# Kernel optimization log

Measured on AMD Instinct MI355X. Metric: run time of the kernel, lower is better.

Reference implementation:

```python
import jax, jax.numpy as jnp
import numpy as np
from jax.ops import segment_sum

N_NODES = 100000
N_EDGES = 1600000
HIDDEN = 128


def gcn_conv(x, src, dst, w, W, b, num_nodes):
    """PyG GCNConv: add self-loops (weight 1), symmetric deg^-1/2 normalization,
    gather from src, scatter-add to dst. x: [N, Fin], W: [Fin, Fout]."""
    loop = jnp.arange(num_nodes, dtype=src.dtype)
    s = jnp.concatenate([src, loop])
    d = jnp.concatenate([dst, loop])
    ww = jnp.concatenate([w, jnp.ones((num_nodes,), dtype=w.dtype)])
    deg = segment_sum(ww, d, num_segments=num_nodes)           # [N]
    dis = jnp.where(deg > 0, jax.lax.rsqrt(jnp.where(deg > 0, deg, 1.0)), 0.0)
    norm = dis[s] * ww * dis[d]                                # [E+N]
    h = x @ W                                                  # [N, Fout]
    msg = norm[:, None] * h[s]                                 # [E+N, Fout]
    out = segment_sum(msg, d, num_segments=num_nodes)          # [N, Fout]
    return out + b


def setup_inputs() -> dict:
    key = jax.random.key(0)
    ks = jax.random.split(key, 12)
    h = HIDDEN
    sc = lambda fan_in: 1.0 / np.sqrt(fan_in)
    return {
        "x": jax.random.normal(ks[0], (N_NODES, 1), dtype=jnp.float32),
        "edge_index": jax.random.randint(ks[1], (2, N_EDGES), 0, N_NODES, dtype=jnp.int64),
        "edge_weight": jax.random.uniform(ks[2], (N_EDGES,), dtype=jnp.float32),
        "W1": jax.random.normal(ks[3], (1, h), dtype=jnp.float32) * sc(1),
        "b1": jnp.zeros((h,), dtype=jnp.float32),
        "W2": jax.random.normal(ks[4], (h, 2 * h), dtype=jnp.float32) * sc(h),
        "b2": jnp.zeros((2 * h,), dtype=jnp.float32),
        "Wl1": jax.random.normal(ks[5], (2 * h, h), dtype=jnp.float32) * sc(2 * h),
        "bl1": jnp.zeros((h,), dtype=jnp.float32),
        "Wl2": jax.random.normal(ks[6], (h, 1), dtype=jnp.float32) * sc(h),
        "bl2": jnp.zeros((1,), dtype=jnp.float32),
    }


def reference(x, edge_index, edge_weight, W1, b1, W2, b2, Wl1, bl1, Wl2, bl2):
    n = x.shape[0]
    src, dst = edge_index[0], edge_index[1]
    h = jax.nn.relu(gcn_conv(x, src, dst, edge_weight, W1, b1, n))
    h = jax.nn.relu(gcn_conv(h, src, dst, edge_weight, W2, b2, n))
    h = jax.nn.relu(h @ Wl1 + bl1)
    return h @ Wl2 + bl2
```

## Files before the change

### kernel.cpp

```cpp
#include <hip/hip_runtime.h>


#define HD 128
#define HD2 256
#define BSHIFT 8
#define BNODES 256
#define SRCBITS 17

typedef __attribute__((ext_vector_type(8))) short bf8_t;
typedef __attribute__((ext_vector_type(4))) float f32x4;

static inline size_t align256(size_t x) { return (x + 255) & ~(size_t)255; }

__device__ inline ushort f2bf(float f) {
    uint u = __float_as_uint(f);
    uint r = u + 0x7fffu + ((u >> 16) & 1u);
    return (ushort)(r >> 16);
}
__device__ inline uint packbf(float a, float b) {
    return (uint)f2bf(a) | ((uint)f2bf(b) << 16);
}

__global__ void k_init(const float* __restrict__ W2, const float* __restrict__ Wl1,
                       ushort* __restrict__ Bt1, ushort* __restrict__ Bt2,
                       int* __restrict__ bfill) {
    int o = blockIdx.x * blockDim.x + threadIdx.x;
    if (o < 512) bfill[o] = 0;
    if (o >= 32768) return;
    {
        int k0 = o & 7, n = (o >> 3) & 255, k8 = o >> 11;
        Bt1[o] = f2bf(W2[(size_t)(k8 * 8 + k0) * 256 + n]);
    }
    {
        int k0 = o & 7, n = (o >> 3) & 127, k8 = o >> 10;
        Bt2[o] = f2bf(Wl1[(size_t)(k8 * 8 + k0) * 128 + n]);
    }
}

__global__ __launch_bounds__(256) void k_part(const int* __restrict__ ei,
                                              const float* __restrict__ ew,
                                              int* __restrict__ bfill,
                                              uint2* __restrict__ stg,
                                              int E, int nbuck, int cap) {
    __shared__ int lcnt[4][512];
    __shared__ int lbase[4][512];
    int tid = threadIdx.x;
    int wvid = tid >> 6;
    for (int i = tid; i < nbuck; i += 256) {
        lcnt[0][i] = 0; lcnt[1][i] = 0; lcnt[2][i] = 0; lcnt[3][i] = 0;
    }
    __syncthreads();
    bool is64 = (ei[1] == 0) && (ei[3] == 0) && (ei[5] == 0) && (ei[7] == 0);
    int e0 = blockIdx.x * 2048;
    uint pack[8]; uint wb[8]; int bkt[8]; int rank[8];
    for (int u = 0; u < 8; u++) {
        int e = e0 + u * 256 + tid;
        bkt[u] = -1;
        if (e < E) {
            int s, d;
            if (is64) { s = ei[2 * e]; d = ei[2 * (E + e)]; }
            else      { s = ei[e];     d = ei[E + e]; }
            bkt[u] = d >> BSHIFT;
            pack[u] = ((uint)(d & (BNODES - 1)) << SRCBITS) | (uint)s;
            wb[u] = __float_as_uint(ew[e]);
            rank[u] = atomicAdd(&lcnt[wvid][bkt[u]], 1);
        }
    }
    __syncthreads();
    for (int i = tid; i < nbuck; i += 256) {
        int t0 = lcnt[0][i], t1 = lcnt[1][i], t2 = lcnt[2][i], t3 = lcnt[3][i];
        int tot = t0 + t1 + t2 + t3;
        int base = tot ? atomicAdd(&bfill[i], tot) : 0;
        lbase[0][i] = base;
        lbase[1][i] = base + t0;
        lbase[2][i] = base + t0 + t1;
        lbase[3][i] = base + t0 + t1 + t2;
    }
    __syncthreads();
    for (int u = 0; u < 8; u++)
        if (bkt[u] >= 0)
            stg[(size_t)bkt[u] * cap + lbase[wvid][bkt[u]] + rank[u]] =
                make_uint2(pack[u], wb[u]);
}

__global__ __launch_bounds__(512) void k_fine(const uint2* __restrict__ stg,
                                              const int* __restrict__ bfill,
                                              const float* __restrict__ x,
                                              float* __restrict__ dis,
                                              float* __restrict__ p,
                                              int* __restrict__ rowptr,
                                              int2* __restrict__ cv,
                                              int cap, int N, int E, int nbuck) {
    __shared__ int cnt_l[BNODES];
    __shared__ int base_l[BNODES];
    __shared__ float degf[BNODES];
    __shared__ int wsum[8];
    int b = blockIdx.x, tid = threadIdx.x;
    int lane = tid & 63, wvid = tid >> 6;
    int a = (tid < b && tid < nbuck) ? bfill[tid] : 0;
    for (int off = 32; off > 0; off >>= 1) a += __shfl_xor(a, off);
    if (lane == 0) wsum[wvid] = a;
    __syncthreads();
    int cb = wsum[0] + wsum[1] + wsum[2] + wsum[3] +
             wsum[4] + wsum[5] + wsum[6] + wsum[7];
    int n = bfill[b];
    if (b == nbuck - 1 && tid == 0) rowptr[N] = E;
    const uint2* s = stg + (size_t)b * cap;
    if (tid < BNODES) { cnt_l[tid] = 0; degf[tid] = 1.0f; }
    __syncthreads();
    for (int i = tid; i < n; i += 512)
        atomicAdd(&cnt_l[s[i].x >> SRCBITS], 1);
    __syncthreads();
    int c = 0;
    if (tid < BNODES) { c = cnt_l[tid]; cnt_l[tid] = 0; }
    int v = c;
    for (int off = 1; off < 64; off <<= 1) {
        int u = __shfl_up(v, off);
        if (lane >= off) v += u;
    }
    if (wvid < 4 && lane == 63) wsum[wvid] = v;
    __syncthreads();
    if (tid < BNODES) {
        int wpre = 0;
        for (int k = 0; k < wvid; k++) wpre += wsum[k];
        base_l[tid] = v + wpre - c;
    }
    __syncthreads();
    for (int i = tid; i < n; i += 512) {
        uint2 r = s[i];
        int dl = r.x >> SRCBITS;
        int src = (int)(r.x & ((1u << SRCBITS) - 1));
        int pos = cb + base_l[dl] + atomicAdd(&cnt_l[dl], 1);
        cv[pos] = make_int2(src, (int)r.y);
        atomicAdd(&degf[dl], __uint_as_float(r.y));
    }
    __syncthreads();
    int gid = (b << BSHIFT) + tid;
    if (tid < BNODES && gid < N) {
        rowptr[gid] = cb + base_l[tid];
        float r = rsqrtf(degf[tid]);
        dis[gid] = r;
        p[gid] = r * x[gid];
    }
}

__global__ __launch_bounds__(256) void k_q(const int* __restrict__ rowptr,
                                           const int2* __restrict__ cv,
                                           const float* __restrict__ dis,
                                           const float* __restrict__ p,
                                           float2* __restrict__ tp, int N) {
    int gid = blockIdx.x * blockDim.x + threadIdx.x;
    int wid = gid >> 4;
    int sl = threadIdx.x & 15;
    if (wid >= N) return;
    int beg = rowptr[wid], end = rowptr[wid + 1];
    float s = 0.0f;
    for (int i = beg + sl; i < end; i += 16) {
        int2 pr = cv[i];
        s += __int_as_float(pr.y) * p[pr.x];
    }
    s += __shfl_xor(s, 1);
    s += __shfl_xor(s, 2);
    s += __shfl_xor(s, 4);
    s += __shfl_xor(s, 8);
    if (sl == 0) {
        float r = dis[wid];
        tp[wid] = make_float2(r * (s + p[wid]), r);
    }
}

__global__ __launch_bounds__(256) void k_agg(const int* __restrict__ rowptr,
                                             const int2* __restrict__ cv,
                                             const float2* __restrict__ tp,
                                             const float* __restrict__ W1,
                                             const float* __restrict__ b1,
                                             uint* __restrict__ z, int N) {
    __shared__ float4 eb[4][32];
    int tid = threadIdx.x;
    int wvid = tid >> 6, lane = tid & 63;
    int wid = (blockIdx.x * blockDim.x + tid) >> 6;
    if (wid >= N) return;
    float2 w1 = *(const float2*)(W1 + lane * 2);
    float2 bb = *(const float2*)(b1 + lane * 2);
    int beg = rowptr[wid], end = rowptr[wid + 1];
    float ax0 = 0.0f, ay0 = 0.0f, ax1 = 0.0f, ay1 = 0.0f;
    for (int base = beg; base < end; base += 64) {
        int eidx = base + lane;
        float wd = 0.0f, tt = 0.0f;
        if (eidx < end) {
            int2 pr = cv[eidx];
            float2 tps = tp[pr.x];
            wd = __int_as_float(pr.y) * tps.y;
            tt = tps.x;
        }
        ((float2*)&eb[wvid][0])[lane] = make_float2(wd, tt);
        int m = min(64, end - base);
        const float4* ebp = &eb[wvid][0];
        int halves = (m + 1) >> 1;
        int u = 0;
        for (; u + 2 <= halves; u += 2) {
            float4 e2 = ebp[u];
            float4 e3 = ebp[u + 1];
            ax0 = fmaf(e2.x, fmaxf(fmaf(e2.y, w1.x, bb.x), 0.0f), ax0);
            ay0 = fmaf(e2.x, fmaxf(fmaf(e2.y, w1.y, bb.y), 0.0f), ay0);
            ax1 = fmaf(e2.z, fmaxf(fmaf(e2.w, w1.x, bb.x), 0.0f), ax1);
            ay1 = fmaf(e2.z, fmaxf(fmaf(e2.w, w1.y, bb.y), 0.0f), ay1);
            ax0 = fmaf(e3.x, fmaxf(fmaf(e3.y, w1.x, bb.x), 0.0f), ax0);
            ay0 = fmaf(e3.x, fmaxf(fmaf(e3.y, w1.y, bb.y), 0.0f), ay0);
            ax1 = fmaf(e3.z, fmaxf(fmaf(e3.w, w1.x, bb.x), 0.0f), ax1);
            ay1 = fmaf(e3.z, fmaxf(fmaf(e3.w, w1.y, bb.y), 0.0f), ay1);
        }
        if (u < halves) {
            float4 e2 = ebp[u];
            ax0 = fmaf(e2.x, fmaxf(fmaf(e2.y, w1.x, bb.x), 0.0f), ax0);
            ay0 = fmaf(e2.x, fmaxf(fmaf(e2.y, w1.y, bb.y), 0.0f), ay0);
            ax1 = fmaf(e2.z, fmaxf(fmaf(e2.w, w1.x, bb.x), 0.0f), ax1);
            ay1 = fmaf(e2.z, fmaxf(fmaf(e2.w, w1.y, bb.y), 0.0f), ay1);
        }
    }
    float ax = ax0 + ax1, ay = ay0 + ay1;
    float2 tpd = tp[wid];
    float rd = tpd.y;
    float s0 = rd * fmaxf(fmaf(tpd.x, w1.x, bb.x), 0.0f);
    float s1 = rd * fmaxf(fmaf(tpd.x, w1.y, bb.y), 0.0f);
    z[(size_t)wid * 64 + lane] = packbf(rd * (ax + s0), rd * (ay + s1));
}

__global__ __launch_bounds__(256) void k_mlp(const ushort* __restrict__ A,
                                             const ushort* __restrict__ Bt1,
                                             const ushort* __restrict__ Bt2,
                                             const float* __restrict__ b2,
                                             const float* __restrict__ bl1,
                                             const float* __restrict__ wl2,
                                             const float* __restrict__ bl2,
                                             float* __restrict__ out, int M) {
    __shared__ ushort st[4][32][40];
    int tid = threadIdx.x;
    int wv = tid >> 6, lane = tid & 63;
    int l15 = lane & 15, quad = lane >> 4;
    int row0 = blockIdx.x * 128 + wv * 32;
    int r0 = row0 + l15;      r0 = r0 < M ? r0 : M - 1;
    int r1 = row0 + 16 + l15; r1 = r1 < M ? r1 : M - 1;

    bf8_t a1[2][4];
    for (int kc = 0; kc < 4; kc++) {
        a1[0][kc] = *(const bf8_t*)(A + (size_t)r0 * 128 + kc * 32 + quad * 8);
        a1[1][kc] = *(const bf8_t*)(A + (size_t)r1 * 128 + kc * 32 + quad * 8);
    }
    f32x4 acc2[2][8];
    for (int i = 0; i < 2; i++)
        for (int j = 0; j < 8; j++) acc2[i][j] = (f32x4){0.f, 0.f, 0.f, 0.f};

    for (int c = 0; c < 8; c++) {
        f32x4 acc1[2][2];
        for (int i = 0; i < 2; i++)
            for (int j = 0; j < 2; j++) acc1[i][j] = (f32x4){0.f, 0.f, 0.f, 0.f};
        for (int kc = 0; kc < 4; kc++)
            for (int nt = 0; nt < 2; nt++) {
                bf8_t b = *(const bf8_t*)(Bt1 +
                    ((size_t)(kc * 4 + quad) * 256 + c * 32 + nt * 16 + l15) * 8);
                acc1[0][nt] = __builtin_amdgcn_mfma_f32_16x16x32_bf16(a1[0][kc], b, acc1[0][nt], 0, 0, 0);
                acc1[1][nt] = __builtin_amdgcn_mfma_f32_16x16x32_bf16(a1[1][kc], b, acc1[1][nt], 0, 0, 0);
            }
        for (int nt = 0; nt < 2; nt++) {
            float bb = b2[c * 32 + nt * 16 + l15];
            for (int mt = 0; mt < 2; mt++)
                for (int rg = 0; rg < 4; rg++)
                    st[wv][mt * 16 + quad * 4 + rg][nt * 16 + l15] =
                        f2bf(fmaxf(acc1[mt][nt][rg] + bb, 0.f));
        }
        bf8_t a2_0 = *(const bf8_t*)&st[wv][l15][quad * 8];
        bf8_t a2_1 = *(const bf8_t*)&st[wv][16 + l15][quad * 8];
        for (int nt2 = 0; nt2 < 8; nt2++) {
            bf8_t b = *(const bf8_t*)(Bt2 +
                ((size_t)(c * 4 + quad) * 128 + nt2 * 16 + l15) * 8);
            acc2[0][nt2] = __builtin_amdgcn_mfma_f32_16x16x32_bf16(a2_0, b, acc2[0][nt2], 0, 0, 0);
            acc2[1][nt2] = __builtin_amdgcn_mfma_f32_16x16x32_bf16(a2_1, b, acc2[1][nt2], 0, 0, 0);
        }
    }
    float rs[2][4] = {};
    for (int nt2 = 0; nt2 < 8; nt2++) {
        int col = nt2 * 16 + l15;
        float bb = bl1[col], ww = wl2[col];
        for (int mt = 0; mt < 2; mt++)
            for (int rg = 0; rg < 4; rg++)
                rs[mt][rg] += fmaxf(acc2[mt][nt2][rg] + bb, 0.f) * ww;
    }
    float base = bl2[0];
    for (int mt = 0; mt < 2; mt++)
        for (int rg = 0; rg < 4; rg++) {
            float s = rs[mt][rg];
            s += __shfl_xor(s, 1);
            s += __shfl_xor(s, 2);
            s += __shfl_xor(s, 4);
            s += __shfl_xor(s, 8);
            int row = row0 + mt * 16 + quad * 4 + rg;
            if (l15 == 0 && row < M) out[row] = s + base;
        }
}

extern "C" void kernel_launch(void* const* d_in, const int* in_sizes, int n_in,
                              void* d_out, int out_size, void* d_ws, size_t ws_size,
                              hipStream_t stream) {
    const float* x   = (const float*)d_in[0];
    const int*   ei  = (const int*)d_in[1];
    const float* ew  = (const float*)d_in[2];
    const float* W1  = (const float*)d_in[3];
    const float* b1  = (const float*)d_in[4];
    const float* W2  = (const float*)d_in[5];
    const float* b2  = (const float*)d_in[6];
    const float* Wl1 = (const float*)d_in[7];
    const float* bl1 = (const float*)d_in[8];
    const float* Wl2 = (const float*)d_in[9];
    const float* bl2 = (const float*)d_in[10];
    float* out = (float*)d_out;
    const int N = in_sizes[0];
    const int E = in_sizes[2];

    const int nbuck = (N + BNODES - 1) >> BSHIFT;
    const int cap = ((E / nbuck) * 5) / 4 + 1024;

    char* w = (char*)d_ws;
    size_t off = 0;
    auto alloc = [&](size_t bytes) -> void* {
        void* p = w + off;
        off = align256(off + bytes);
        return p;
    };
    uint*   z      = (uint*)alloc((size_t)N * 64 * 4);
    float2* tp     = (float2*)alloc((size_t)N * 8);
    float*  dis    = (float*)alloc((size_t)N * 4);
    float*  p_     = (float*)alloc((size_t)N * 4);
    int*    rowptr = (int*)alloc((size_t)(N + 1) * 4);
    int2*   cv     = (int2*)alloc((size_t)E * 8);
    uint2*  stg    = (uint2*)alloc((size_t)nbuck * cap * 8);
    int*    bfill  = (int*)alloc(512 * 4);
    ushort* Bt1    = (ushort*)alloc(32768 * 2);
    ushort* Bt2    = (ushort*)alloc(32768 * 2);

    k_init<<<128, 256, 0, stream>>>(W2, Wl1, Bt1, Bt2, bfill);
    k_part<<<(E + 2047) / 2048, 256, 0, stream>>>(ei, ew, bfill, stg, E, nbuck, cap);
    k_fine<<<nbuck, 512, 0, stream>>>(stg, bfill, x, dis, p_, rowptr, cv, cap, N, E, nbuck);
    k_q<<<(N * 16 + 255) / 256, 256, 0, stream>>>(rowptr, cv, dis, p_, tp, N);
    k_agg<<<(N + 3) / 4, 256, 0, stream>>>(rowptr, cv, tp, W1, b1, z, N);
    k_mlp<<<(N + 127) / 128, 256, 0, stream>>>((const ushort*)z, Bt1, Bt2,
                                               b2, bl1, Wl2, bl2, out, N);
}
```

Baseline: 212.6 us.

## Fuse second-layer aggregation into MLP kernel via swizzled shared-memory tile

```diff
diff --git a/kernel.cpp b/kernel.cpp
--- a/kernel.cpp
+++ b/kernel.cpp
@@ -169,83 +169,80 @@
     }
 }
 
-__global__ __launch_bounds__(256) void k_agg(const int* __restrict__ rowptr,
-                                             const int2* __restrict__ cv,
-                                             const float2* __restrict__ tp,
-                                             const float* __restrict__ W1,
-                                             const float* __restrict__ b1,
-                                             uint* __restrict__ z, int N) {
+__global__ __launch_bounds__(256, 3) void k_aggmlp(
+        const int* __restrict__ rowptr, const int2* __restrict__ cv,
+        const float2* __restrict__ tp,
+        const float* __restrict__ W1, const float* __restrict__ b1,
+        const ushort* __restrict__ Bt1,
+        const ushort* __restrict__ Bt2,
+        const float* __restrict__ b2, const float* __restrict__ bl1,
+        const float* __restrict__ wl2, const float* __restrict__ bl2,
+        float* __restrict__ out, int M) {
+    __shared__ uint   zs[4][32][64];
+    __shared__ ushort st[4][32][40];
     __shared__ float4 eb[4][32];
-    int tid = threadIdx.x;
-    int wvid = tid >> 6, lane = tid & 63;
-    int wid = (blockIdx.x * blockDim.x + tid) >> 6;
-    if (wid >= N) return;
-    float2 w1 = *(const float2*)(W1 + lane * 2);
-    float2 bb = *(const float2*)(b1 + lane * 2);
-    int beg = rowptr[wid], end = rowptr[wid + 1];
-    float ax0 = 0.0f, ay0 = 0.0f, ax1 = 0.0f, ay1 = 0.0f;
-    for (int base = beg; base < end; base += 64) {
-        int eidx = base + lane;
-        float wd = 0.0f, tt = 0.0f;
-        if (eidx < end) {
-            int2 pr = cv[eidx];
-            float2 tps = tp[pr.x];
-            wd = __int_as_float(pr.y) * tps.y;
-            tt = tps.x;
-        }
-        ((float2*)&eb[wvid][0])[lane] = make_float2(wd, tt);
-        int m = min(64, end - base);
-        const float4* ebp = &eb[wvid][0];
-        int halves = (m + 1) >> 1;
-        int u = 0;
-        for (; u + 2 <= halves; u += 2) {
-            float4 e2 = ebp[u];
-            float4 e3 = ebp[u + 1];
-            ax0 = fmaf(e2.x, fmaxf(fmaf(e2.y, w1.x, bb.x), 0.0f), ax0);
-            ay0 = fmaf(e2.x, fmaxf(fmaf(e2.y, w1.y, bb.y), 0.0f), ay0);
-            ax1 = fmaf(e2.z, fmaxf(fmaf(e2.w, w1.x, bb.x), 0.0f), ax1);
-            ay1 = fmaf(e2.z, fmaxf(fmaf(e2.w, w1.y, bb.y), 0.0f), ay1);
-            ax0 = fmaf(e3.x, fmaxf(fmaf(e3.y, w1.x, bb.x), 0.0f), ax0);
-            ay0 = fmaf(e3.x, fmaxf(fmaf(e3.y, w1.y, bb.y), 0.0f), ay0);
-            ax1 = fmaf(e3.z, fmaxf(fmaf(e3.w, w1.x, bb.x), 0.0f), ax1);
-            ay1 = fmaf(e3.z, fmaxf(fmaf(e3.w, w1.y, bb.y), 0.0f), ay1);
-        }
-        if (u < halves) {
-            float4 e2 = ebp[u];
-            ax0 = fmaf(e2.x, fmaxf(fmaf(e2.y, w1.x, bb.x), 0.0f), ax0);
-            ay0 = fmaf(e2.x, fmaxf(fmaf(e2.y, w1.y, bb.y), 0.0f), ay0);
-            ax1 = fmaf(e2.z, fmaxf(fmaf(e2.w, w1.x, bb.x), 0.0f), ax1);
-            ay1 = fmaf(e2.z, fmaxf(fmaf(e2.w, w1.y, bb.y), 0.0f), ay1);
-        }
-    }
-    float ax = ax0 + ax1, ay = ay0 + ay1;
-    float2 tpd = tp[wid];
-    float rd = tpd.y;
-    float s0 = rd * fmaxf(fmaf(tpd.x, w1.x, bb.x), 0.0f);
-    float s1 = rd * fmaxf(fmaf(tpd.x, w1.y, bb.y), 0.0f);
-    z[(size_t)wid * 64 + lane] = packbf(rd * (ax + s0), rd * (ay + s1));
-}
-
-__global__ __launch_bounds__(256) void k_mlp(const ushort* __restrict__ A,
-                                             const ushort* __restrict__ Bt1,
-                                             const ushort* __restrict__ Bt2,
-                                             const float* __restrict__ b2,
-                                             const float* __restrict__ bl1,
-                                             const float* __restrict__ wl2,
-                                             const float* __restrict__ bl2,
-                                             float* __restrict__ out, int M) {
-    __shared__ ushort st[4][32][40];
     int tid = threadIdx.x;
     int wv = tid >> 6, lane = tid & 63;
     int l15 = lane & 15, quad = lane >> 4;
     int row0 = blockIdx.x * 128 + wv * 32;
-    int r0 = row0 + l15;      r0 = r0 < M ? r0 : M - 1;
-    int r1 = row0 + 16 + l15; r1 = r1 < M ? r1 : M - 1;
+    float2 w1 = *(const float2*)(W1 + lane * 2);
+    float2 bb1 = *(const float2*)(b1 + lane * 2);
+
+    for (int i = 0; i < 32; i++) {
+        int node = row0 + i;
+        uint pk = 0u;
+        if (node < M) {
+            int beg = rowptr[node], end = rowptr[node + 1];
+            float ax0 = 0.0f, ay0 = 0.0f, ax1 = 0.0f, ay1 = 0.0f;
+            for (int base = beg; base < end; base += 64) {
+                int eidx = base + lane;
+                float wd = 0.0f, tt = 0.0f;
+                if (eidx < end) {
+                    int2 pr = cv[eidx];
+                    float2 tps = tp[pr.x];
+                    wd = __int_as_float(pr.y) * tps.y;
+                    tt = tps.x;
+                }
+                ((float2*)&eb[wv][0])[lane] = make_float2(wd, tt);
+                int m = min(64, end - base);
+                const float4* ebp = &eb[wv][0];
+                int halves = (m + 1) >> 1;
+                int u = 0;
+                for (; u + 2 <= halves; u += 2) {
+                    float4 e2 = ebp[u];
+                    float4 e3 = ebp[u + 1];
+                    ax0 = fmaf(e2.x, fmaxf(fmaf(e2.y, w1.x, bb1.x), 0.0f), ax0);
+                    ay0 = fmaf(e2.x, fmaxf(fmaf(e2.y, w1.y, bb1.y), 0.0f), ay0);
+                    ax1 = fmaf(e2.z, fmaxf(fmaf(e2.w, w1.x, bb1.x), 0.0f), ax1);
+                    ay1 = fmaf(e2.z, fmaxf(fmaf(e2.w, w1.y, bb1.y), 0.0f), ay1);
+                    ax0 = fmaf(e3.x, fmaxf(fmaf(e3.y, w1.x, bb1.x), 0.0f), ax0);
+                    ay0 = fmaf(e3.x, fmaxf(fmaf(e3.y, w1.y, bb1.y), 0.0f), ay0);
+                    ax1 = fmaf(e3.z, fmaxf(fmaf(e3.w, w1.x, bb1.x), 0.0f), ax1);
+                    ay1 = fmaf(e3.z, fmaxf(fmaf(e3.w, w1.y, bb1.y), 0.0f), ay1);
+                }
+                if (u < halves) {
+                    float4 e2 = ebp[u];
+                    ax0 = fmaf(e2.x, fmaxf(fmaf(e2.y, w1.x, bb1.x), 0.0f), ax0);
+                    ay0 = fmaf(e2.x, fmaxf(fmaf(e2.y, w1.y, bb1.y), 0.0f), ay0);
+                    ax1 = fmaf(e2.z, fmaxf(fmaf(e2.w, w1.x, bb1.x), 0.0f), ax1);
+                    ay1 = fmaf(e2.z, fmaxf(fmaf(e2.w, w1.y, bb1.y), 0.0f), ay1);
+                }
+            }
+            float ax = ax0 + ax1, ay = ay0 + ay1;
+            float2 tpd = tp[node];
+            float rd = tpd.y;
+            float s0 = rd * fmaxf(fmaf(tpd.x, w1.x, bb1.x), 0.0f);
+            float s1 = rd * fmaxf(fmaf(tpd.x, w1.y, bb1.y), 0.0f);
+            pk = packbf(rd * (ax + s0), rd * (ay + s1));
+        }
+        zs[wv][i][((((uint)lane >> 2) ^ (uint)(i & 15)) << 2) | (lane & 3)] = pk;
+    }
 
     bf8_t a1[2][4];
     for (int kc = 0; kc < 4; kc++) {
-        a1[0][kc] = *(const bf8_t*)(A + (size_t)r0 * 128 + kc * 32 + quad * 8);
-        a1[1][kc] = *(const bf8_t*)(A + (size_t)r1 * 128 + kc * 32 + quad * 8);
+        uint ga = (uint)(kc * 4 + quad) ^ (uint)l15;
+        a1[0][kc] = *(const bf8_t*)&zs[wv][l15][ga << 2];
+        a1[1][kc] = *(const bf8_t*)&zs[wv][16 + l15][ga << 2];
     }
     f32x4 acc2[2][8];
     for (int i = 0; i < 2; i++)
@@ -327,7 +324,6 @@
         off = align256(off + bytes);
         return p;
     };
-    uint*   z      = (uint*)alloc((size_t)N * 64 * 4);
     float2* tp     = (float2*)alloc((size_t)N * 8);
     float*  dis    = (float*)alloc((size_t)N * 4);
     float*  p_     = (float*)alloc((size_t)N * 4);
@@ -342,7 +338,7 @@
     k_part<<<(E + 2047) / 2048, 256, 0, stream>>>(ei, ew, bfill, stg, E, nbuck, cap);
     k_fine<<<nbuck, 512, 0, stream>>>(stg, bfill, x, dis, p_, rowptr, cv, cap, N, E, nbuck);
     k_q<<<(N * 16 + 255) / 256, 256, 0, stream>>>(rowptr, cv, dis, p_, tp, N);
-    k_agg<<<(N + 3) / 4, 256, 0, stream>>>(rowptr, cv, tp, W1, b1, z, N);
-    k_mlp<<<(N + 127) / 128, 256, 0, stream>>>((const ushort*)z, Bt1, Bt2,
-                                               b2, bl1, Wl2, bl2, out, N);
-}
+    k_aggmlp<<<(N + 127) / 128, 256, 0, stream>>>(rowptr, cv, tp, W1, b1,
+                                                  Bt1, Bt2, b2, bl1, Wl2, bl2,
+                                                  out, N);
+}
```

New measurement: 257.3 us. +21.0%, slower.

## Replace bucketed two-pass CSR build with global atomic count-scan-scatter

Applied to the files above, without the earlier changes.

```diff
diff --git a/kernel.cpp b/kernel.cpp
--- a/kernel.cpp
+++ b/kernel.cpp
@@ -3,9 +3,6 @@
 
 #define HD 128
 #define HD2 256
-#define BSHIFT 8
-#define BNODES 256
-#define SRCBITS 17
 
 typedef __attribute__((ext_vector_type(8))) short bf8_t;
 typedef __attribute__((ext_vector_type(4))) float f32x4;
@@ -23,10 +20,9 @@
 
 __global__ void k_init(const float* __restrict__ W2, const float* __restrict__ Wl1,
                        ushort* __restrict__ Bt1, ushort* __restrict__ Bt2,
-                       int* __restrict__ bfill) {
+                       int* __restrict__ cnt, float* __restrict__ degw, int NP) {
     int o = blockIdx.x * blockDim.x + threadIdx.x;
-    if (o < 512) bfill[o] = 0;
-    if (o >= 32768) return;
+    for (int i = o; i < NP; i += 32768) { cnt[i] = 0; degw[i] = 1.0f; }
     {
         int k0 = o & 7, n = (o >> 3) & 255, k8 = o >> 11;
         Bt1[o] = f2bf(W2[(size_t)(k8 * 8 + k0) * 256 + n]);
@@ -37,111 +33,78 @@
     }
 }
 
-__global__ __launch_bounds__(256) void k_part(const int* __restrict__ ei,
-                                              const float* __restrict__ ew,
-                                              int* __restrict__ bfill,
-                                              uint2* __restrict__ stg,
-                                              int E, int nbuck, int cap) {
-    __shared__ int lcnt[4][512];
-    __shared__ int lbase[4][512];
+__global__ __launch_bounds__(256) void k_count(const int* __restrict__ ei,
+                                               const float* __restrict__ ew,
+                                               int* __restrict__ cnt,
+                                               float* __restrict__ degw, int E) {
+    int e = blockIdx.x * 256 + threadIdx.x;
+    if (e >= E) return;
+    bool is64 = (ei[1] == 0) && (ei[3] == 0) && (ei[5] == 0) && (ei[7] == 0);
+    int d = is64 ? ei[2 * (E + e)] : ei[E + e];
+    atomicAdd(&cnt[d], 1);
+    atomicAdd(&degw[d], ew[e]);
+}
+
+__global__ __launch_bounds__(256) void k_scan1(const int* __restrict__ cnt,
+                                               int* __restrict__ bsum) {
+    __shared__ int ws[4];
     int tid = threadIdx.x;
-    int wvid = tid >> 6;
-    for (int i = tid; i < nbuck; i += 256) {
-        lcnt[0][i] = 0; lcnt[1][i] = 0; lcnt[2][i] = 0; lcnt[3][i] = 0;
-    }
+    int v = cnt[blockIdx.x * 256 + tid];
+    for (int off = 32; off > 0; off >>= 1) v += __shfl_xor(v, off);
+    if ((tid & 63) == 0) ws[tid >> 6] = v;
     __syncthreads();
-    bool is64 = (ei[1] == 0) && (ei[3] == 0) && (ei[5] == 0) && (ei[7] == 0);
-    int e0 = blockIdx.x * 2048;
-    uint pack[8]; uint wb[8]; int bkt[8]; int rank[8];
-    for (int u = 0; u < 8; u++) {
-        int e = e0 + u * 256 + tid;
-        bkt[u] = -1;
-        if (e < E) {
-            int s, d;
-            if (is64) { s = ei[2 * e]; d = ei[2 * (E + e)]; }
-            else      { s = ei[e];     d = ei[E + e]; }
-            bkt[u] = d >> BSHIFT;
-            pack[u] = ((uint)(d & (BNODES - 1)) << SRCBITS) | (uint)s;
-            wb[u] = __float_as_uint(ew[e]);
-            rank[u] = atomicAdd(&lcnt[wvid][bkt[u]], 1);
-        }
-    }
+    if (tid == 0) bsum[blockIdx.x] = ws[0] + ws[1] + ws[2] + ws[3];
+}
+
+__global__ __launch_bounds__(256) void k_scan2(const int* __restrict__ cnt,
+                                               const int* __restrict__ bsum,
+                                               const float* __restrict__ degw,
+                                               const float* __restrict__ x,
+                                               int* __restrict__ rowptr,
+                                               float* __restrict__ dis,
+                                               float* __restrict__ p, int N) {
+    __shared__ int ws[4], ws2[4];
+    int b = blockIdx.x, tid = threadIdx.x;
+    int lane = tid & 63, wv = tid >> 6;
+    int a = (tid < b) ? bsum[tid] : 0;
+    if (tid + 256 < b) a += bsum[tid + 256];
+    for (int off = 32; off > 0; off >>= 1) a += __shfl_xor(a, off);
+    if (lane == 0) ws[wv] = a;
     __syncthreads();
-    for (int i = tid; i < nbuck; i += 256) {
-        int t0 = lcnt[0][i], t1 = lcnt[1][i], t2 = lcnt[2][i], t3 = lcnt[3][i];
-        int tot = t0 + t1 + t2 + t3;
-        int base = tot ? atomicAdd(&bfill[i], tot) : 0;
-        lbase[0][i] = base;
-        lbase[1][i] = base + t0;
-        lbase[2][i] = base + t0 + t1;
-        lbase[3][i] = base + t0 + t1 + t2;
-    }
-    __syncthreads();
-    for (int u = 0; u < 8; u++)
-        if (bkt[u] >= 0)
-            stg[(size_t)bkt[u] * cap + lbase[wvid][bkt[u]] + rank[u]] =
-                make_uint2(pack[u], wb[u]);
-}
-
-__global__ __launch_bounds__(512) void k_fine(const uint2* __restrict__ stg,
-                                              const int* __restrict__ bfill,
-                                              const float* __restrict__ x,
-                                              float* __restrict__ dis,
-                                              float* __restrict__ p,
-                                              int* __restrict__ rowptr,
-                                              int2* __restrict__ cv,
-                                              int cap, int N, int E, int nbuck) {
-    __shared__ int cnt_l[BNODES];
-    __shared__ int base_l[BNODES];
-    __shared__ float degf[BNODES];
-    __shared__ int wsum[8];
-    int b = blockIdx.x, tid = threadIdx.x;
-    int lane = tid & 63, wvid = tid >> 6;
-    int a = (tid < b && tid < nbuck) ? bfill[tid] : 0;
-    for (int off = 32; off > 0; off >>= 1) a += __shfl_xor(a, off);
-    if (lane == 0) wsum[wvid] = a;
-    __syncthreads();
-    int cb = wsum[0] + wsum[1] + wsum[2] + wsum[3] +
-             wsum[4] + wsum[5] + wsum[6] + wsum[7];
-    int n = bfill[b];
-    if (b == nbuck - 1 && tid == 0) rowptr[N] = E;
-    const uint2* s = stg + (size_t)b * cap;
-    if (tid < BNODES) { cnt_l[tid] = 0; degf[tid] = 1.0f; }
-    __syncthreads();
-    for (int i = tid; i < n; i += 512)
-        atomicAdd(&cnt_l[s[i].x >> SRCBITS], 1);
-    __syncthreads();
-    int c = 0;
-    if (tid < BNODES) { c = cnt_l[tid]; cnt_l[tid] = 0; }
+    int cb = ws[0] + ws[1] + ws[2] + ws[3];
+    int gid = b * 256 + tid;
+    int c = cnt[gid];
     int v = c;
     for (int off = 1; off < 64; off <<= 1) {
         int u = __shfl_up(v, off);
         if (lane >= off) v += u;
     }
-    if (wvid < 4 && lane == 63) wsum[wvid] = v;
+    if (lane == 63) ws2[wv] = v;
     __syncthreads();
-    if (tid < BNODES) {
-        int wpre = 0;
-        for (int k = 0; k < wvid; k++) wpre += wsum[k];
-        base_l[tid] = v + wpre - c;
-    }
-    __syncthreads();
-    for (int i = tid; i < n; i += 512) {
-        uint2 r = s[i];
-        int dl = r.x >> SRCBITS;
-        int src = (int)(r.x & ((1u << SRCBITS) - 1));
-        int pos = cb + base_l[dl] + atomicAdd(&cnt_l[dl], 1);
-        cv[pos] = make_int2(src, (int)r.y);
-        atomicAdd(&degf[dl], __uint_as_float(r.y));
-    }
-    __syncthreads();
-    int gid = (b << BSHIFT) + tid;
-    if (tid < BNODES && gid < N) {
-        rowptr[gid] = cb + base_l[tid];
-        float r = rsqrtf(degf[tid]);
+    int wpre = 0;
+    for (int k = 0; k < wv; k++) wpre += ws2[k];
+    if (gid <= N) rowptr[gid] = cb + wpre + v - c;
+    if (gid < N) {
+        float r = rsqrtf(degw[gid]);
         dis[gid] = r;
         p[gid] = r * x[gid];
     }
+}
+
+__global__ __launch_bounds__(256) void k_scatter(const int* __restrict__ ei,
+                                                 const float* __restrict__ ew,
+                                                 const int* __restrict__ rowptr,
+                                                 int* __restrict__ cnt,
+                                                 int2* __restrict__ cv, int E) {
+    int e = blockIdx.x * 256 + threadIdx.x;
+    if (e >= E) return;
+    bool is64 = (ei[1] == 0) && (ei[3] == 0) && (ei[5] == 0) && (ei[7] == 0);
+    int s, d;
+    if (is64) { s = ei[2 * e]; d = ei[2 * (E + e)]; }
+    else      { s = ei[e];     d = ei[E + e]; }
+    float w0 = ew[e];
+    int slot = atomicSub(&cnt[d], 1) - 1;
+    cv[rowptr[d] + slot] = make_int2(s, __float_as_int(w0));
 }
 
 __global__ __launch_bounds__(256) void k_q(const int* __restrict__ rowptr,
@@ -317,8 +280,8 @@
     const int N = in_sizes[0];
     const int E = in_sizes[2];
 
-    const int nbuck = (N + BNODES - 1) >> BSHIFT;
-    const int cap = ((E / nbuck) * 5) / 4 + 1024;
+    const int NBLK = N / 256 + 1;
+    const int NP = NBLK * 256;
 
     char* w = (char*)d_ws;
     size_t off = 0;
@@ -333,14 +296,17 @@
     float*  p_     = (float*)alloc((size_t)N * 4);
     int*    rowptr = (int*)alloc((size_t)(N + 1) * 4);
     int2*   cv     = (int2*)alloc((size_t)E * 8);
-    uint2*  stg    = (uint2*)alloc((size_t)nbuck * cap * 8);
-    int*    bfill  = (int*)alloc(512 * 4);
+    int*    cnt    = (int*)alloc((size_t)NP * 4);
+    float*  degw   = (float*)alloc((size_t)NP * 4);
+    int*    bsum   = (int*)alloc(512 * 4);
     ushort* Bt1    = (ushort*)alloc(32768 * 2);
     ushort* Bt2    = (ushort*)alloc(32768 * 2);
 
-    k_init<<<128, 256, 0, stream>>>(W2, Wl1, Bt1, Bt2, bfill);
-    k_part<<<(E + 2047) / 2048, 256, 0, stream>>>(ei, ew, bfill, stg, E, nbuck, cap);
-    k_fine<<<nbuck, 512, 0, stream>>>(stg, bfill, x, dis, p_, rowptr, cv, cap, N, E, nbuck);
+    k_init<<<128, 256, 0, stream>>>(W2, Wl1, Bt1, Bt2, cnt, degw, NP);
+    k_count<<<(E + 255) / 256, 256, 0, stream>>>(ei, ew, cnt, degw, E);
+    k_scan1<<<NBLK, 256, 0, stream>>>(cnt, bsum);
+    k_scan2<<<NBLK, 256, 0, stream>>>(cnt, bsum, degw, x, rowptr, dis, p_, N);
+    k_scatter<<<(E + 255) / 256, 256, 0, stream>>>(ei, ew, rowptr, cnt, cv, E);
     k_q<<<(N * 16 + 255) / 256, 256, 0, stream>>>(rowptr, cv, dis, p_, tp, N);
     k_agg<<<(N + 3) / 4, 256, 0, stream>>>(rowptr, cv, tp, W1, b1, z, N);
     k_mlp<<<(N + 127) / 128, 256, 0, stream>>>((const ushort*)z, Bt1, Bt2,
```

Result: slower. 406.6 us (+91.2%).
